# Performance work log

Measured on AMD Instinct MI355X. Metric: run time of the kernel, lower is better.

Reference implementation:

```python
import jax, jax.numpy as jnp
import numpy as np

V, D, NH, L, T, B = 32000, 1024, 16, 6, 1024, 2
HS = D // NH
EPS = 1e-5


def setup_inputs() -> dict:
    key = jax.random.key(0)
    ks = jax.random.split(key, 20)
    s = 0.02
    inp = {
        'tokens': jax.random.randint(ks[0], (B, T), 0, V),
        'tok_emb': jax.random.normal(ks[1], (V, D), jnp.float32) * s,
        'pos_emb': jax.random.normal(ks[2], (T, D), jnp.float32) * s,
        'Wq': jax.random.normal(ks[3], (L, D, NH, HS), jnp.float32) * s,
        'Wk': jax.random.normal(ks[4], (L, D, NH, HS), jnp.float32) * s,
        'Wv': jax.random.normal(ks[5], (L, D, NH, HS), jnp.float32) * s,
        'Wo': jax.random.normal(ks[6], (L, D, D), jnp.float32) * s,
        'bo': jnp.zeros((L, D), jnp.float32),
        'ln1_s': jnp.ones((L, D), jnp.float32),
        'ln1_b': jnp.zeros((L, D), jnp.float32),
        'ln2_s': jnp.ones((L, D), jnp.float32),
        'ln2_b': jnp.zeros((L, D), jnp.float32),
        'W1': jax.random.normal(ks[7], (L, D, 4 * D), jnp.float32) * s,
        'b1': jnp.zeros((L, 4 * D), jnp.float32),
        'W2': jax.random.normal(ks[8], (L, 4 * D, D), jnp.float32) * s,
        'b2': jnp.zeros((L, D), jnp.float32),
        'lnf_s': jnp.ones((D,), jnp.float32),
        'lnf_b': jnp.zeros((D,), jnp.float32),
        'Wlm': jax.random.normal(ks[9], (D, V), jnp.float32) * s,
        'blm': jnp.zeros((V,), jnp.float32),
    }
    return inp


def _layernorm(x, scale, bias):
    m = jnp.mean(x, axis=-1, keepdims=True)
    v = jnp.mean(jnp.square(x - m), axis=-1, keepdims=True)
    return (x - m) * jax.lax.rsqrt(v + EPS) * scale + bias


def reference(tokens, tok_emb, pos_emb, Wq, Wk, Wv, Wo, bo,
              ln1_s, ln1_b, ln2_s, ln2_b, W1, b1, W2, b2,
              lnf_s, lnf_b, Wlm, blm):
    x = tok_emb[tokens] + pos_emb[None, :, :]  # [B,T,D]
    causal = jnp.tril(jnp.ones((T, T), bool))
    scale = HS ** -0.5
    for l in range(L):
        h = _layernorm(x, ln1_s[l], ln1_b[l])
        q = jnp.einsum('btd,dhe->bhte', h, Wq[l])
        k = jnp.einsum('btd,dhe->bhte', h, Wk[l])
        v = jnp.einsum('btd,dhe->bhte', h, Wv[l])
        wei = jnp.einsum('bhqe,bhke->bhqk', q, k) * scale
        wei = jnp.where(causal, wei, -jnp.inf)
        wei = jax.nn.softmax(wei, axis=-1)
        attn = jnp.einsum('bhqk,bhke->bhqe', wei, v)  # [B,NH,T,HS]
        attn = attn.transpose(0, 2, 1, 3).reshape(B, T, D)
        x = x + attn @ Wo[l] + bo[l]
        h = _layernorm(x, ln2_s[l], ln2_b[l])
        x = x + jax.nn.relu(h @ W1[l] + b1[l]) @ W2[l] + b2[l]
    x = _layernorm(x, lnf_s, lnf_b)
    logits = x @ Wlm + blm  # [B,T,V]
    return logits
```

## Files before the change

### kernel.cpp

```cpp
#include <hip/hip_runtime.h>
#include <hip/hip_bf16.h>
#include <stdint.h>

#define L_LAYERS 6
#define D_MODEL  1024
#define N_HEAD   16
#define H_SZ     64
#define T_SEQ    1024
#define B_BATCH  2
#define M_ROWS   2048
#define V_VOCAB  32000

typedef __attribute__((ext_vector_type(8))) short bf16x8;
typedef __attribute__((ext_vector_type(4))) short bf16x4;
typedef __attribute__((ext_vector_type(4))) float floatx4;

static __device__ __forceinline__ short f2bf(float f) {
  __hip_bfloat16 h = __float2bfloat16(f);
  return *reinterpret_cast<short*>(&h);
}
static __device__ __forceinline__ float bf2f(short s) {
  unsigned u = ((unsigned)(unsigned short)s) << 16;
  return *reinterpret_cast<float*>(&u);
}

static __device__ __forceinline__ void lds_cp16(const void* g, void* l) {
  __builtin_amdgcn_global_load_lds(
      (const __attribute__((address_space(1))) uint32_t*)g,
      (__attribute__((address_space(3))) uint32_t*)l, 16, 0, 0);
}

#define WVM(n) asm volatile("s_waitcnt vmcnt(" #n ")" ::: "memory")
#define BARR __builtin_amdgcn_s_barrier()

__global__ __launch_bounds__(256) void transpose_cvt(const float* __restrict__ in,
                                                     short* __restrict__ out,
                                                     int R, int C,
                                                     long in_stride, long out_stride) {
  in  += (size_t)blockIdx.z * in_stride;
  out += (size_t)blockIdx.z * out_stride;
  __shared__ float tile[64][65];
  int rt = blockIdx.x, ct = blockIdx.y;
  int tid = threadIdx.x;
  int r0 = tid >> 4;
  int c0 = (tid & 15) << 2;
  const float* ip = in + (size_t)(rt * 64) * C + ct * 64;
#pragma unroll
  for (int p = 0; p < 4; ++p) {
    int r = r0 + (p << 4);
    float4 v = *(const float4*)(ip + (size_t)r * C + c0);
    tile[r][c0] = v.x; tile[r][c0 + 1] = v.y; tile[r][c0 + 2] = v.z; tile[r][c0 + 3] = v.w;
  }
  __syncthreads();
  short* op = out + (size_t)(ct * 64) * R + rt * 64;
#pragma unroll
  for (int p = 0; p < 2; ++p) {
    int c = (tid >> 3) + (p << 5);
    int r8 = (tid & 7) << 3;
    bf16x8 o8;
#pragma unroll
    for (int j = 0; j < 8; ++j) o8[j] = f2bf(tile[r8 + j][c]);
    *(bf16x8*)(op + (size_t)c * R + r8) = o8;
  }
}

__global__ __launch_bounds__(256) void embedln_kernel(const int* __restrict__ tokens,
                                                      const float* __restrict__ tok_emb,
                                                      const float* __restrict__ pos_emb,
                                                      float* __restrict__ x,
                                                      const float* __restrict__ sc,
                                                      const float* __restrict__ bi,
                                                      short* __restrict__ out) {
  int row = blockIdx.x, tid = threadIdx.x;
  int t = row & 1023;
  int tok = tokens[row];
  int c = tid << 2;
  float4 e = *(const float4*)(tok_emb + (size_t)tok * 1024 + c);
  float4 p = *(const float4*)(pos_emb + (size_t)t * 1024 + c);
  float4 v; v.x = e.x + p.x; v.y = e.y + p.y; v.z = e.z + p.z; v.w = e.w + p.w;
  *(float4*)(x + (size_t)row * 1024 + c) = v;
  float s = v.x + v.y + v.z + v.w;
  float q = v.x * v.x + v.y * v.y + v.z * v.z + v.w * v.w;
#pragma unroll
  for (int off = 32; off > 0; off >>= 1) {
    s += __shfl_xor(s, off);
    q += __shfl_xor(q, off);
  }
  __shared__ float rs[4], rq[4];
  if ((tid & 63) == 0) { rs[tid >> 6] = s; rq[tid >> 6] = q; }
  __syncthreads();
  s = rs[0] + rs[1] + rs[2] + rs[3];
  q = rq[0] + rq[1] + rq[2] + rq[3];
  float mean = s * (1.f / 1024.f);
  float var = q * (1.f / 1024.f) - mean * mean;
  float rstd = rsqrtf(var + 1e-5f);
  float4 g = *(const float4*)(sc + c);
  float4 bb = *(const float4*)(bi + c);
  bf16x4 o4;
  o4.x = f2bf((v.x - mean) * rstd * g.x + bb.x);
  o4.y = f2bf((v.y - mean) * rstd * g.y + bb.y);
  o4.z = f2bf((v.z - mean) * rstd * g.z + bb.z);
  o4.w = f2bf((v.w - mean) * rstd * g.w + bb.w);
  *(bf16x4*)(out + (size_t)row * 1024 + c) = o4;
}

__global__ __launch_bounds__(256) void lnred_kernel(float* __restrict__ xio,
                                                    const short* __restrict__ P0,
                                                    const short* __restrict__ P1,
                                                    const float* __restrict__ gb,
                                                    const float* __restrict__ sc,
                                                    const float* __restrict__ bi,
                                                    short* __restrict__ out) {
  int row = blockIdx.x, tid = threadIdx.x;
  int c = tid << 2;
  size_t base = (size_t)row * 1024 + c;
  float4 v = *(const float4*)(xio + base);
  bf16x4 p0 = *(const bf16x4*)(P0 + base);
  bf16x4 p1 = *(const bf16x4*)(P1 + base);
  float4 gv = *(const float4*)(gb + c);
  v.x += bf2f(p0.x) + bf2f(p1.x) + gv.x;
  v.y += bf2f(p0.y) + bf2f(p1.y) + gv.y;
  v.z += bf2f(p0.z) + bf2f(p1.z) + gv.z;
  v.w += bf2f(p0.w) + bf2f(p1.w) + gv.w;
  *(float4*)(xio + base) = v;
  float s = v.x + v.y + v.z + v.w;
  float q = v.x * v.x + v.y * v.y + v.z * v.z + v.w * v.w;
#pragma unroll
  for (int off = 32; off > 0; off >>= 1) {
    s += __shfl_xor(s, off);
    q += __shfl_xor(q, off);
  }
  __shared__ float rs[4], rq[4];
  if ((tid & 63) == 0) { rs[tid >> 6] = s; rq[tid >> 6] = q; }
  __syncthreads();
  s = rs[0] + rs[1] + rs[2] + rs[3];
  q = rq[0] + rq[1] + rq[2] + rq[3];
  float mean = s * (1.f / 1024.f);
  float var = q * (1.f / 1024.f) - mean * mean;
  float rstd = rsqrtf(var + 1e-5f);
  float4 g = *(const float4*)(sc + c);
  float4 bb = *(const float4*)(bi + c);
  bf16x4 o4;
  o4.x = f2bf((v.x - mean) * rstd * g.x + bb.x);
  o4.y = f2bf((v.y - mean) * rstd * g.y + bb.y);
  o4.z = f2bf((v.z - mean) * rstd * g.z + bb.z);
  o4.w = f2bf((v.w - mean) * rstd * g.w + bb.w);
  *(bf16x4*)(out + (size_t)row * 1024 + c) = o4;
}

__global__ __launch_bounds__(256) void lnred4_kernel(float* __restrict__ xio,
                                                     const short* __restrict__ P01,
                                                     const short* __restrict__ P23,
                                                     const float* __restrict__ gb,
                                                     const float* __restrict__ sc,
                                                     const float* __restrict__ bi,
                                                     short* __restrict__ out) {
  const size_t MN = (size_t)M_ROWS * 1024;
  int row = blockIdx.x, tid = threadIdx.x;
  int c = tid << 2;
  size_t base = (size_t)row * 1024 + c;
  float4 v = *(const float4*)(xio + base);
  bf16x4 p0 = *(const bf16x4*)(P01 + base);
  bf16x4 p1 = *(const bf16x4*)(P01 + MN + base);
  bf16x4 p2 = *(const bf16x4*)(P23 + base);
  bf16x4 p3 = *(const bf16x4*)(P23 + MN + base);
  float4 gv = *(const float4*)(gb + c);
  v.x += bf2f(p0.x) + bf2f(p1.x) + bf2f(p2.x) + bf2f(p3.x) + gv.x;
  v.y += bf2f(p0.y) + bf2f(p1.y) + bf2f(p2.y) + bf2f(p3.y) + gv.y;
  v.z += bf2f(p0.z) + bf2f(p1.z) + bf2f(p2.z) + bf2f(p3.z) + gv.z;
  v.w += bf2f(p0.w) + bf2f(p1.w) + bf2f(p2.w) + bf2f(p3.w) + gv.w;
  *(float4*)(xio + base) = v;
  float s = v.x + v.y + v.z + v.w;
  float q = v.x * v.x + v.y * v.y + v.z * v.z + v.w * v.w;
#pragma unroll
  for (int off = 32; off > 0; off >>= 1) {
    s += __shfl_xor(s, off);
    q += __shfl_xor(q, off);
  }
  __shared__ float rs[4], rq[4];
  if ((tid & 63) == 0) { rs[tid >> 6] = s; rq[tid >> 6] = q; }
  __syncthreads();
  s = rs[0] + rs[1] + rs[2] + rs[3];
  q = rq[0] + rq[1] + rq[2] + rq[3];
  float mean = s * (1.f / 1024.f);
  float var = q * (1.f / 1024.f) - mean * mean;
  float rstd = rsqrtf(var + 1e-5f);
  float4 g = *(const float4*)(sc + c);
  float4 bb = *(const float4*)(bi + c);
  bf16x4 o4;
  o4.x = f2bf((v.x - mean) * rstd * g.x + bb.x);
  o4.y = f2bf((v.y - mean) * rstd * g.y + bb.y);
  o4.z = f2bf((v.z - mean) * rstd * g.z + bb.z);
  o4.w = f2bf((v.w - mean) * rstd * g.w + bb.w);
  *(bf16x4*)(out + (size_t)row * 1024 + c) = o4;
}

__global__ __launch_bounds__(256) void gemm3sk_kernel(const short* __restrict__ A,
                                                      const short* __restrict__ Bt,
                                                      short* __restrict__ Pout,
                                                      int K, int N) {
  constexpr int ABY = 64 * 128;
  constexpr int BBY = 128 * 128;
  extern __shared__ char smem[];
  char* Asm = smem;
  char* Bsm = smem + 3 * ABY;
  const int NB = N >> 7;
  int nwg = 64 * NB;
  int bid = blockIdx.x;
  int wgid = (bid & 7) * (nwg >> 3) + (bid >> 3);
  int half = wgid >= (nwg >> 1);
  int w2 = wgid - half * (nwg >> 1);
  int bn = w2 >> 5, bm = w2 & 31;
  int kbase = half * (K >> 1);
  Pout += (size_t)half * M_ROWS * N;
  int tid = threadIdx.x;
  int lane = tid & 63, w = tid >> 6;
  int lr = lane & 15, lg = lane >> 4;
  int wn = w & 1, wm = w >> 1;

  const floatx4 FZ = {0.f, 0.f, 0.f, 0.f};
  floatx4 acc[2][4];
#pragma unroll
  for (int m = 0; m < 2; ++m)
#pragma unroll
    for (int n = 0; n < 4; ++n) acc[m][n] = FZ;

  size_t aoff[2], boff[4];
  {
    int rr = tid >> 3;
    int g = (tid & 7) ^ (rr & 7);
#pragma unroll
    for (int i = 0; i < 2; ++i)
      aoff[i] = (size_t)(bm * 64 + i * 32 + rr) * K + kbase + g * 8;
#pragma unroll
    for (int i = 0; i < 4; ++i)
      boff[i] = (size_t)(bn * 128 + i * 32 + rr) * K + kbase + g * 8;
  }

#define STA3(b, k0)                                                        \
  _Pragma("unroll") for (int i = 0; i < 2; ++i)                            \
    lds_cp16(A + aoff[i] + (k0), Asm + (b) * ABY + i * 4096 + tid * 16);
#define STB3(b, k0)                                                        \
  _Pragma("unroll") for (int i = 0; i < 4; ++i)                            \
    lds_cp16(Bt + boff[i] + (k0), Bsm + (b) * BBY + i * 4096 + tid * 16);
#define LDA3(b, kh)                                                        \
  _Pragma("unroll") for (int f = 0; f < 2; ++f) {                          \
    int lrow = wm * 32 + f * 16 + lr;                                      \
    af[f] = *(const bf16x8*)(Asm + (b) * ABY + lrow * 128 +                \
                             (((((kh) << 2) + lg) ^ (lrow & 7)) << 4));    \
  }
#define LDB3(b, kh)                                                        \
  _Pragma("unroll") for (int n = 0; n < 4; ++n) {                          \
    int lcol = wn * 64 + n * 16 + lr;                                      \
    bfr[n] = *(const bf16x8*)(Bsm + (b) * BBY + lcol * 128 +               \
                              (((((kh) << 2) + lg) ^ (lcol & 7)) << 4));   \
  }
#define MFMA3                                                              \
  __builtin_amdgcn_s_setprio(1);                                           \
  _Pragma("unroll") for (int f = 0; f < 2; ++f)                            \
  _Pragma("unroll") for (int n = 0; n < 4; ++n)                            \
    acc[f][n] = __builtin_amdgcn_mfma_f32_16x16x32_bf16(af[f], bfr[n],     \
                                                        acc[f][n], 0, 0, 0);\
  __builtin_amdgcn_s_setprio(0);

  const int nt = (K >> 1) >> 6;
  STA3(0, 0); STB3(0, 0);
  STA3(1, 64); STB3(1, 64);
  WVM(6);
  BARR;

  int cbuf = 0, sbuf = 2;
  for (int t = 0; t < nt; ++t) {
    bf16x8 af[2], bfr[4];
    bool pre = (t + 2 < nt);
    int k2 = (t + 2) << 6;
    if (pre) { STA3(sbuf, k2); }
    LDA3(cbuf, 0); LDB3(cbuf, 0);
    MFMA3;
    if (pre) { STB3(sbuf, k2); }
    LDA3(cbuf, 1); LDB3(cbuf, 1);
    MFMA3;
    if (pre) { WVM(6); } else { WVM(0); }
    BARR;
    cbuf = (cbuf == 2) ? 0 : cbuf + 1;
    sbuf = (sbuf == 2) ? 0 : sbuf + 1;
  }

#pragma unroll
  for (int n = 0; n < 4; ++n) {
    int col = (bn << 7) + wn * 64 + (n << 4) + lr;
#pragma unroll
    for (int m = 0; m < 2; ++m) {
      int row0 = bm * 64 + wm * 32 + (m << 4) + (lg << 2);
#pragma unroll
      for (int r = 0; r < 4; ++r)
        Pout[(size_t)(row0 + r) * N + col] = f2bf(acc[m][n][r]);
    }
  }
#undef STA3
#undef STB3
#undef LDA3
#undef LDB3
#undef MFMA3
}

template <bool BIAS, bool RELU, bool OUTBF16, bool VSPLIT>
__global__ __launch_bounds__(512) void gemmw_kernel(const short* __restrict__ A,
                                                    const short* __restrict__ Bt,
                                                    const float* __restrict__ bias,
                                                    void* __restrict__ Cout,
                                                    short* __restrict__ vtb,
                                                    int K, int N) {
  constexpr int ABY = 128 * 128;
  constexpr int BBY = 256 * 128;
  extern __shared__ char smem[];
  char* Asm = smem;
  char* Bsm = smem + 3 * ABY;
  const int NB = N >> 8;
  int nwg = 16 * NB;
  int bid = blockIdx.x;
  int wgid = (bid & 7) * (nwg >> 3) + (bid >> 3);
  int bn = wgid >> 4, bm = wgid & 15;
  int tid = threadIdx.x;
  int lane = tid & 63, w = tid >> 6;
  int lr = lane & 15, lg = lane >> 4;
  int wm = w >> 2, wn = w & 3;

  const floatx4 FZ = {0.f, 0.f, 0.f, 0.f};
  floatx4 acc[4][4];
#pragma unroll
  for (int m = 0; m < 4; ++m)
#pragma unroll
    for (int n = 0; n < 4; ++n) acc[m][n] = FZ;

  size_t aoff[2], boff[4];
  {
    int rr = tid >> 3;
    int g = (tid & 7) ^ (rr & 7);
#pragma unroll
    for (int i = 0; i < 2; ++i)
      aoff[i] = (size_t)(bm * 128 + i * 64 + rr) * K + g * 8;
#pragma unroll
    for (int i = 0; i < 4; ++i)
      boff[i] = (size_t)(bn * 256 + i * 64 + rr) * K + g * 8;
  }

#define STAW(b, k0)                                                        \
  _Pragma("unroll") for (int i = 0; i < 2; ++i)                            \
    lds_cp16(A + aoff[i] + (k0), Asm + (b) * ABY + i * 8192 + tid * 16);
#define STBW(b, k0)                                                        \
  _Pragma("unroll") for (int i = 0; i < 4; ++i)                            \
    lds_cp16(Bt + boff[i] + (k0), Bsm + (b) * BBY + i * 8192 + tid * 16);
#define LDAW(b, kh)                                                        \
  _Pragma("unroll") for (int f = 0; f < 4; ++f) {                          \
    int lrow = wm * 64 + f * 16 + lr;                                      \
    af[f] = *(const bf16x8*)(Asm + (b) * ABY + lrow * 128 +                \
                             (((((kh) << 2) + lg) ^ (lrow & 7)) << 4));    \
  }
#define LDBW(b, kh)                                                        \
  _Pragma("unroll") for (int n = 0; n < 4; ++n) {                          \
    int lcol = wn * 64 + n * 16 + lr;                                      \
    bfr[n] = *(const bf16x8*)(Bsm + (b) * BBY + lcol * 128 +               \
                              (((((kh) << 2) + lg) ^ (lcol & 7)) << 4));   \
  }
#define MFMAW                                                              \
  __builtin_amdgcn_s_setprio(1);                                           \
  _Pragma("unroll") for (int f = 0; f < 4; ++f)                            \
  _Pragma("unroll") for (int n = 0; n < 4; ++n)                            \
    acc[f][n] = __builtin_amdgcn_mfma_f32_16x16x32_bf16(af[f], bfr[n],     \
                                                        acc[f][n], 0, 0, 0);\
  __builtin_amdgcn_s_setprio(0);

  const int nt = K >> 6;
  STAW(0, 0); STBW(0, 0);
  STAW(1, 64); STBW(1, 64);
  WVM(6);
  BARR;

  int cbuf = 0, sbuf = 2;
  for (int t = 0; t < nt; ++t) {
    bf16x8 af[4], bfr[4];
    bool pre = (t + 2 < nt);
    int k2 = (t + 2) << 6;
    if (pre) { STAW(sbuf, k2); }
    LDAW(cbuf, 0); LDBW(cbuf, 0);
    MFMAW;
    if (pre) { STBW(sbuf, k2); }
    LDAW(cbuf, 1); LDBW(cbuf, 1);
    MFMAW;
    if (pre) { WVM(6); } else { WVM(0); }
    BARR;
    cbuf = (cbuf == 2) ? 0 : cbuf + 1;
    sbuf = (sbuf == 2) ? 0 : sbuf + 1;
  }

#pragma unroll
  for (int n = 0; n < 4; ++n) {
    int col = (bn << 8) + wn * 64 + (n << 4) + lr;
    float bv = 0.f;
    if (BIAS) bv = bias[col];
#pragma unroll
    for (int m = 0; m < 4; ++m) {
      int row0 = bm * 128 + wm * 64 + (m << 4) + (lg << 2);
      if (VSPLIT && col >= 2048) {
        int hc = col - 2048;
        int brow = row0 >> 10, t0 = row0 & 1023;
        ushort4 pk;
        pk.x = (unsigned short)f2bf(acc[m][n][0]);
        pk.y = (unsigned short)f2bf(acc[m][n][1]);
        pk.z = (unsigned short)f2bf(acc[m][n][2]);
        pk.w = (unsigned short)f2bf(acc[m][n][3]);
        *(ushort4*)(vtb + ((size_t)(((brow << 4) + (hc >> 6)) << 6) + (hc & 63)) * 1024 + t0) = pk;
      } else {
#pragma unroll
        for (int r = 0; r < 4; ++r) {
          size_t idx = (size_t)(row0 + r) * N + col;
          float val = acc[m][n][r] + bv;
          if (RELU) val = fmaxf(val, 0.f);
          if (OUTBF16) ((short*)Cout)[idx] = f2bf(val);
          else ((float*)Cout)[idx] = val;
        }
      }
    }
  }
#undef STAW
#undef STBW
#undef LDAW
#undef LDBW
#undef MFMAW
}

__global__ __launch_bounds__(512) void gemmwsk_kernel(const short* __restrict__ A,
                                                      const short* __restrict__ Bt,
                                                      short* __restrict__ P01,
                                                      short* __restrict__ P23,
                                                      int K, int N) {
  constexpr int ABY = 128 * 128;
  constexpr int BBY = 256 * 128;
  extern __shared__ char smem[];
  char* Asm = smem;
  char* Bsm = smem + 3 * ABY;
  const int NB = N >> 8;
  int nwg = 16 * NB * 4;
  int bid = blockIdx.x;
  int wgid = (bid & 7) * (nwg >> 3) + (bid >> 3);
  int per = nwg >> 2;
  int part = wgid / per;
  int w2 = wgid - part * per;
  int bn = w2 >> 4, bm = w2 & 15;
  int kbase = part * (K >> 2);
  short* Pout = (part < 2 ? P01 + (size_t)part * M_ROWS * N
                          : P23 + (size_t)(part - 2) * M_ROWS * N);
  int tid = threadIdx.x;
  int lane = tid & 63, w = tid >> 6;
  int lr = lane & 15, lg = lane >> 4;
  int wm = w >> 2, wn = w & 3;

  const floatx4 FZ = {0.f, 0.f, 0.f, 0.f};
  floatx4 acc[4][4];
#pragma unroll
  for (int m = 0; m < 4; ++m)
#pragma unroll
    for (int n = 0; n < 4; ++n) acc[m][n] = FZ;

  size_t aoff[2], boff[4];
  {
    int rr = tid >> 3;
    int g = (tid & 7) ^ (rr & 7);
#pragma unroll
    for (int i = 0; i < 2; ++i)
      aoff[i] = (size_t)(bm * 128 + i * 64 + rr) * K + kbase + g * 8;
#pragma unroll
    for (int i = 0; i < 4; ++i)
      boff[i] = (size_t)(bn * 256 + i * 64 + rr) * K + kbase + g * 8;
  }

#define STAW(b, k0)                                                        \
  _Pragma("unroll") for (int i = 0; i < 2; ++i)                            \
    lds_cp16(A + aoff[i] + (k0), Asm + (b) * ABY + i * 8192 + tid * 16);
#define STBW(b, k0)                                                        \
  _Pragma("unroll") for (int i = 0; i < 4; ++i)                            \
    lds_cp16(Bt + boff[i] + (k0), Bsm + (b) * BBY + i * 8192 + tid * 16);
#define LDAW(b, kh)                                                        \
  _Pragma("unroll") for (int f = 0; f < 4; ++f) {                          \
    int lrow = wm * 64 + f * 16 + lr;                                      \
    af[f] = *(const bf16x8*)(Asm + (b) * ABY + lrow * 128 +                \
                             (((((kh) << 2) + lg) ^ (lrow & 7)) << 4));    \
  }
#define LDBW(b, kh)                                                        \
  _Pragma("unroll") for (int n = 0; n < 4; ++n) {                          \
    int lcol = wn * 64 + n * 16 + lr;                                      \
    bfr[n] = *(const bf16x8*)(Bsm + (b) * BBY + lcol * 128 +               \
                              (((((kh) << 2) + lg) ^ (lcol & 7)) << 4));   \
  }
#define MFMAW                                                              \
  __builtin_amdgcn_s_setprio(1);                                           \
  _Pragma("unroll") for (int f = 0; f < 4; ++f)                            \
  _Pragma("unroll") for (int n = 0; n < 4; ++n)                            \
    acc[f][n] = __builtin_amdgcn_mfma_f32_16x16x32_bf16(af[f], bfr[n],     \
                                                        acc[f][n], 0, 0, 0);\
  __builtin_amdgcn_s_setprio(0);

  const int nt = (K >> 2) >> 6;
  STAW(0, 0); STBW(0, 0);
  STAW(1, 64); STBW(1, 64);
  WVM(6);
  BARR;

  int cbuf = 0, sbuf = 2;
  for (int t = 0; t < nt; ++t) {
    bf16x8 af[4], bfr[4];
    bool pre = (t + 2 < nt);
    int k2 = (t + 2) << 6;
    if (pre) { STAW(sbuf, k2); }
    LDAW(cbuf, 0); LDBW(cbuf, 0);
    MFMAW;
    if (pre) { STBW(sbuf, k2); }
    LDAW(cbuf, 1); LDBW(cbuf, 1);
    MFMAW;
    if (pre) { WVM(6); } else { WVM(0); }
    BARR;
    cbuf = (cbuf == 2) ? 0 : cbuf + 1;
    sbuf = (sbuf == 2) ? 0 : sbuf + 1;
  }

#pragma unroll
  for (int n = 0; n < 4; ++n) {
    int col = (bn << 8) + wn * 64 + (n << 4) + lr;
#pragma unroll
    for (int m = 0; m < 4; ++m) {
      int row0 = bm * 128 + wm * 64 + (m << 4) + (lg << 2);
#pragma unroll
      for (int r = 0; r < 4; ++r)
        Pout[(size_t)(row0 + r) * N + col] = f2bf(acc[m][n][r]);
    }
  }
#undef STAW
#undef STBW
#undef LDAW
#undef LDBW
#undef MFMAW
}

template <bool BIAS, bool OUTBF16>
__global__ __launch_bounds__(512) void gemm8_kernel(const short* __restrict__ A,
                                                    const short* __restrict__ Bt,
                                                    const float* __restrict__ bias,
                                                    void* __restrict__ Cout,
                                                    int K, int N) {
  extern __shared__ char smem[];
  char* Asm = smem;
  char* Bsm = smem + 65536;
  const int NB = N >> 8;
  int nwg = 8 * NB;
  int bid = blockIdx.x;
  int wgid = (bid & 7) * (nwg >> 3) + (bid >> 3);
  int bm = wgid & 7, bn = wgid >> 3;
  int tid = threadIdx.x;
  int lane = tid & 63, w = tid >> 6;
  int lr = lane & 15, lg = lane >> 4;
  int wm = w >> 2, wn = w & 3;

  const floatx4 FZ = {0.f, 0.f, 0.f, 0.f};
  floatx4 acc[8][4];
#pragma unroll
  for (int m = 0; m < 8; ++m)
#pragma unroll
    for (int n = 0; n < 4; ++n) acc[m][n] = FZ;

  size_t aoff[2][2], boff[4];
  {
    int rr = tid >> 3;
    int g = (tid & 7) ^ (rr & 7);
#pragma unroll
    for (int c = 0; c < 2; ++c)
#pragma unroll
      for (int i = 0; i < 2; ++i) {
        int lrow = i * 64 + rr;
        int grow = (lrow & 63) + ((lrow >> 6) << 7) + (c << 6);
        aoff[c][i] = (size_t)(bm * 256 + grow) * K + g * 8;
      }
#pragma unroll
    for (int i = 0; i < 4; ++i)
      boff[i] = (size_t)(bn * 256 + i * 64 + rr) * K + g * 8;
  }

  bf16x8 areg[4], breg[2][4];

#define LDA8(chunk, kh)                                                          \
  _Pragma("unroll") for (int f = 0; f < 4; ++f) {                                \
    int lrow = wm * 64 + f * 16 + lr;                                            \
    areg[f] = *(const bf16x8*)(Asm + buf * 32768 + (chunk) * 16384 + lrow * 128  \
                               + (((((kh) << 2) + lg) ^ (lrow & 7)) << 4));      \
  }
#define LDB8(kh)                                                                 \
  _Pragma("unroll") for (int n = 0; n < 4; ++n) {                                \
    int lcol = wn * 64 + n * 16 + lr;                                            \
    breg[kh][n] = *(const bf16x8*)(Bsm + buf * 32768 + lcol * 128                \
                                   + (((((kh) << 2) + lg) ^ (lcol & 7)) << 4));  \
  }
#define MFMA16(mh, kh)                                                           \
  __builtin_amdgcn_s_setprio(1);                                                 \
  _Pragma("unroll") for (int f = 0; f < 4; ++f)                                  \
  _Pragma("unroll") for (int n = 0; n < 4; ++n)                                  \
    acc[(mh) * 4 + f][n] = __builtin_amdgcn_mfma_f32_16x16x32_bf16(              \
        areg[f], breg[kh][n], acc[(mh) * 4 + f][n], 0, 0, 0);                    \
  __builtin_amdgcn_s_setprio(0);
#define STA8(chunk, dstbuf, k0)                                                  \
  _Pragma("unroll") for (int i = 0; i < 2; ++i)                                  \
    lds_cp16(A + aoff[chunk][i] + (k0),                                          \
             Asm + (dstbuf) * 32768 + (chunk) * 16384 + i * 8192 + tid * 16);
#define STB8(dstbuf, k0)                                                         \
  _Pragma("unroll") for (int i = 0; i < 4; ++i)                                  \
    lds_cp16(Bt + boff[i] + (k0),                                                \
             Bsm + (dstbuf) * 32768 + i * 8192 + tid * 16);

  const int nt = K >> 6;
  STA8(0, 0, 0); STB8(0, 0); STA8(1, 0, 0);
  WVM(2);
  BARR;

  int buf = 0;
  for (int t = 0; t < nt - 1; ++t) {
    int k1 = (t + 1) << 6;
    int ob = buf ^ 1;
    LDA8(0, 0); LDB8(0);
    STA8(0, ob, k1);
    BARR;
    MFMA16(0, 0);
    BARR;
    LDA8(0, 1); LDB8(1);
    STB8(ob, k1);
    WVM(6);
    BARR;
    MFMA16(0, 1);
    BARR;
    LDA8(1, 0);
    STA8(1, ob, k1);
    BARR;
    MFMA16(1, 0);
    BARR;
    LDA8(1, 1);
    WVM(2);
    BARR;
    MFMA16(1, 1);
    BARR;
    buf ^= 1;
  }
  LDA8(0, 0); LDB8(0);
  MFMA16(0, 0);
  LDA8(0, 1); LDB8(1);
  MFMA16(0, 1);
  WVM(0);
  BARR;
  LDA8(1, 0);
  MFMA16(1, 0);
  LDA8(1, 1);
  MFMA16(1, 1);

#pragma unroll
  for (int n = 0; n < 4; ++n) {
    int col = (bn << 8) + (wn << 6) + (n << 4) + lr;
    float bv = 0.f;
    if (BIAS) bv = bias[col];
#pragma unroll
    for (int m = 0; m < 8; ++m) {
      int row0 = (bm << 8) + (wm << 7) + (m << 4) + (lg << 2);
#pragma unroll
      for (int r = 0; r < 4; ++r) {
        size_t idx = (size_t)(row0 + r) * N + col;
        float val = acc[m][n][r] + bv;
        if (OUTBF16) ((short*)Cout)[idx] = f2bf(val);
        else ((float*)Cout)[idx] = val;
      }
    }
  }
#undef LDA8
#undef LDB8
#undef MFMA16
#undef STA8
#undef STB8
}

__global__ __launch_bounds__(256) void attn_kernel(const short* __restrict__ qkv,
                                                   const short* __restrict__ vt,
                                                   short* __restrict__ out) {
  int bh = blockIdx.x;
  int qt = blockIdx.y;
  int b = bh >> 4, hh = bh & 15;
  int tid = threadIdx.x;
  int lane = tid & 63, w = tid >> 6;
  int lr = lane & 15, lg = lane >> 4;

  __shared__ short Ks[128 * 64];
  __shared__ short Vs[64 * 128];
  __shared__ short Ps[4][16 * 132];

  const floatx4 FZ = {0.f, 0.f, 0.f, 0.f};
  const float C2 = 0.18033688f;
  const short* qb = qkv + (size_t)((b << 10) + (qt << 6) + (w << 4) + lr) * 3072 + (hh << 6);
  bf16x8 qf0 = *(const bf16x8*)(qb + (lg << 3));
  bf16x8 qf1 = *(const bf16x8*)(qb + 32 + (lg << 3));

  floatx4 o[4];
  float mrun[4], lrun[4];
#pragma unroll
  for (int r = 0; r < 4; ++r) { o[r] = FZ; mrun[r] = -3e38f; lrun[r] = 0.f; }

  int krow = tid >> 3, kgr = tid & 7;
  int vrow = tid >> 4, vgr = tid & 15;
  const short* kB = qkv + (size_t)(b << 10) * 3072 + 1024 + (hh << 6);
  const short* vB = vt + (size_t)(bh << 6) * 1024;

#define STKV(JT)                                                           \
  _Pragma("unroll") for (int i = 0; i < 4; ++i) {                          \
    int r = (i << 5) + krow;                                               \
    lds_cp16(kB + (size_t)(((JT) << 7) + r) * 3072 + ((kgr ^ (r & 7)) << 3), \
             (char*)Ks + i * 4096 + tid * 16);                             \
  }                                                                        \
  _Pragma("unroll") for (int i = 0; i < 4; ++i) {                          \
    int r = (i << 4) + vrow;                                               \
    lds_cp16(vB + (size_t)r * 1024 + ((JT) << 7) + ((vgr ^ (r & 15)) << 3), \
             (char*)Vs + i * 4096 + tid * 16);                             \
  }

#define CHUNK_COMPUTE(NF, MASK, JT)                                        \
  {                                                                        \
    const char* KsB = (const char*)Ks;                                     \
    const char* VsB = (const char*)Vs;                                     \
    floatx4 s[NF];                                                         \
    _Pragma("unroll") for (int f = 0; f < NF; ++f) {                       \
      int rk = (f << 4) + lr;                                              \
      int sw = rk & 7;                                                     \
      bf16x8 kf0 = *(const bf16x8*)(KsB + rk * 128 + ((lg ^ sw) << 4));    \
      bf16x8 kf1 = *(const bf16x8*)(KsB + rk * 128 + (((4 + lg) ^ sw) << 4)); \
      floatx4 t0 = __builtin_amdgcn_mfma_f32_16x16x32_bf16(qf0, kf0, FZ, 0, 0, 0); \
      s[f] = __builtin_amdgcn_mfma_f32_16x16x32_bf16(qf1, kf1, t0, 0, 0, 0); \
    }                                                                      \
    int qrow0 = (qt << 6) + (w << 4) + (lg << 2);                          \
    _Pragma("unroll") for (int f = 0; f < NF; ++f)                         \
    _Pragma("unroll") for (int r = 0; r < 4; ++r) {                        \
      float sv = s[f][r] * C2;                                             \
      if (MASK && (((JT) << 7) + (f << 4) + lr > qrow0 + r)) sv = -3e38f;  \
      s[f][r] = sv;                                                        \
    }                                                                      \
    float mt[4] = {-3e38f, -3e38f, -3e38f, -3e38f};                        \
    _Pragma("unroll") for (int f = 0; f < NF; ++f)                         \
    _Pragma("unroll") for (int r = 0; r < 4; ++r) mt[r] = fmaxf(mt[r], s[f][r]); \
    _Pragma("unroll") for (int off = 1; off < 16; off <<= 1)               \
    _Pragma("unroll") for (int r = 0; r < 4; ++r)                          \
      mt[r] = fmaxf(mt[r], __shfl_xor(mt[r], off));                        \
    float corr[4], psum[4];                                                \
    _Pragma("unroll") for (int r = 0; r < 4; ++r) {                        \
      float mnew = fmaxf(mrun[r], mt[r]);                                  \
      corr[r] = exp2f(mrun[r] - mnew);                                     \
      mrun[r] = mnew;                                                      \
      float ps = 0.f;                                                      \
      _Pragma("unroll") for (int f = 0; f < NF; ++f) {                     \
        float e = exp2f(s[f][r] - mnew);                                   \
        s[f][r] = e;                                                       \
        ps += e;                                                           \
      }                                                                    \
      psum[r] = ps;                                                        \
    }                                                                      \
    _Pragma("unroll") for (int off = 1; off < 16; off <<= 1)               \
    _Pragma("unroll") for (int r = 0; r < 4; ++r)                          \
      psum[r] += __shfl_xor(psum[r], off);                                 \
    floatx4 cv;                                                            \
    _Pragma("unroll") for (int r = 0; r < 4; ++r) {                        \
      lrun[r] = lrun[r] * corr[r] + psum[r];                               \
      cv[r] = corr[r];                                                     \
    }                                                                      \
    _Pragma("unroll") for (int f = 0; f < 4; ++f) o[f] *= cv;              \
    char* PsB = (char*)&Ps[w][0];                                          \
    _Pragma("unroll") for (int f = 0; f < NF; ++f)                         \
    _Pragma("unroll") for (int r = 0; r < 4; ++r)                          \
      *(short*)(PsB + ((lg << 2) + r) * 264 + (((f << 4) + lr) << 1)) =    \
          f2bf(s[f][r]);                                                   \
    _Pragma("unroll") for (int kk = 0; kk < (NF >> 1); ++kk) {             \
      const char* pb = PsB + lr * 264 + (kk << 6) + (lg << 4);             \
      union { struct { bf16x4 lo, hi; } h2; bf16x8 v; } pu;                \
      pu.h2.lo = *(const bf16x4*)pb;                                       \
      pu.h2.hi = *(const bf16x4*)(pb + 8);                                 \
      bf16x8 pa = pu.v;                                                    \
      _Pragma("unroll") for (int f = 0; f < 4; ++f) {                      \
        int rv = (f << 4) + lr;                                            \
        bf16x8 vf = *(const bf16x8*)(VsB + rv * 256 +                      \
                                     ((((kk << 2) + lg) ^ (rv & 15)) << 4)); \
        o[f] = __builtin_amdgcn_mfma_f32_16x16x32_bf16(pa, vf, o[f], 0, 0, 0); \
      }                                                                    \
    }                                                                      \
  }

  const int nfull = qt >> 1;
  for (int jt = 0; jt < nfull; ++jt) {
    STKV(jt);
    WVM(0);
    BARR;
    CHUNK_COMPUTE(8, false, jt)
    BARR;
  }
  STKV(nfull);
  WVM(0);
  BARR;
  if (qt & 1) {
    CHUNK_COMPUTE(8, true, nfull)
  } else {
    CHUNK_COMPUTE(4, true, nfull)
  }
#undef STKV
#undef CHUNK_COMPUTE

#pragma unroll
  for (int f = 0; f < 4; ++f) {
#pragma unroll
    for (int r = 0; r < 4; ++r) {
      int row = (qt << 6) + (w << 4) + (lg << 2) + r;
      int col = (hh << 6) + (f << 4) + lr;
      out[(size_t)((b << 10) + row) * 1024 + col] = f2bf(o[f][r] / lrun[r]);
    }
  }
}

extern "C" void kernel_launch(void* const* d_in, const int* in_sizes, int n_in,
                              void* d_out, int out_size, void* d_ws, size_t ws_size,
                              hipStream_t stream) {
  const int*   tokens  = (const int*)d_in[0];
  const float* tok_emb = (const float*)d_in[1];
  const float* pos_emb = (const float*)d_in[2];
  const float* Wq  = (const float*)d_in[3];
  const float* Wk  = (const float*)d_in[4];
  const float* Wv  = (const float*)d_in[5];
  const float* Wo  = (const float*)d_in[6];
  const float* bo  = (const float*)d_in[7];
  const float* ln1s = (const float*)d_in[8];
  const float* ln1b = (const float*)d_in[9];
  const float* ln2s = (const float*)d_in[10];
  const float* ln2b = (const float*)d_in[11];
  const float* W1  = (const float*)d_in[12];
  const float* b1  = (const float*)d_in[13];
  const float* W2  = (const float*)d_in[14];
  const float* b2  = (const float*)d_in[15];
  const float* lnfs = (const float*)d_in[16];
  const float* lnfb = (const float*)d_in[17];
  const float* Wlm = (const float*)d_in[18];
  const float* blm = (const float*)d_in[19];

  short* wqkvT = (short*)d_ws;
  short* woT   = wqkvT + (size_t)L_LAYERS * 3072 * 1024;
  short* w1T   = woT   + (size_t)L_LAYERS * 1024 * 1024;
  short* w2T   = w1T   + (size_t)L_LAYERS * 4096 * 1024;
  short* wlmT  = w2T   + (size_t)L_LAYERS * 1024 * 4096;
  float* x     = (float*)(wlmT + (size_t)V_VOCAB * 1024);
  short* h     = (short*)(x + (size_t)M_ROWS * 1024);
  short* qkv   = h + (size_t)M_ROWS * 1024;
  short* vtb   = qkv + (size_t)M_ROWS * 3072;
  short* attnb = vtb + (size_t)B_BATCH * N_HEAD * H_SZ * T_SEQ;
  short* mid   = attnb + (size_t)M_ROWS * 1024;
  short* psum  = mid + (size_t)M_ROWS * 4096;
  short* psum1 = psum + (size_t)M_ROWS * 1024;
  short* psum23 = qkv;

  dim3 blk(256, 1, 1);

  (void)hipFuncSetAttribute(reinterpret_cast<const void*>(&gemm8_kernel<true, false>),
                            hipFuncAttributeMaxDynamicSharedMemorySize, 131072);
  (void)hipFuncSetAttribute(reinterpret_cast<const void*>(&gemm3sk_kernel),
                            hipFuncAttributeMaxDynamicSharedMemorySize, 73728);
  (void)hipFuncSetAttribute(reinterpret_cast<const void*>(&gemmw_kernel<false, false, true, true>),
                            hipFuncAttributeMaxDynamicSharedMemorySize, 147456);
  (void)hipFuncSetAttribute(reinterpret_cast<const void*>(&gemmw_kernel<true, true, true, false>),
                            hipFuncAttributeMaxDynamicSharedMemorySize, 147456);
  (void)hipFuncSetAttribute(reinterpret_cast<const void*>(&gemmwsk_kernel),
                            hipFuncAttributeMaxDynamicSharedMemorySize, 147456);

  transpose_cvt<<<dim3(16, 16, 6), blk, 0, stream>>>(Wq, wqkvT,             1024, 1024, 1048576, 3072 * 1024);
  transpose_cvt<<<dim3(16, 16, 6), blk, 0, stream>>>(Wk, wqkvT + 1048576,   1024, 1024, 1048576, 3072 * 1024);
  transpose_cvt<<<dim3(16, 16, 6), blk, 0, stream>>>(Wv, wqkvT + 2097152,   1024, 1024, 1048576, 3072 * 1024);
  transpose_cvt<<<dim3(16, 16, 6), blk, 0, stream>>>(Wo, woT,               1024, 1024, 1048576, 1048576);
  transpose_cvt<<<dim3(16, 64, 6), blk, 0, stream>>>(W1, w1T,               1024, 4096, 4194304, 4194304);
  transpose_cvt<<<dim3(64, 16, 6), blk, 0, stream>>>(W2, w2T,               4096, 1024, 4194304, 4194304);
  transpose_cvt<<<dim3(16, 500, 1), blk, 0, stream>>>(Wlm, wlmT,            1024, V_VOCAB, 0, 0);

  embedln_kernel<<<M_ROWS, blk, 0, stream>>>(tokens, tok_emb, pos_emb, x, ln1s, ln1b, h);

  for (int l = 0; l < L_LAYERS; ++l) {
    if (l > 0) {
      lnred4_kernel<<<M_ROWS, blk, 0, stream>>>(x, psum, psum23, b2 + (l - 1) * 1024,
                                                ln1s + l * 1024, ln1b + l * 1024, h);
    }
    gemmw_kernel<false, false, true, true><<<16 * 12, dim3(512, 1, 1), 147456, stream>>>(
        h, wqkvT + (size_t)l * 3072 * 1024, nullptr, qkv, vtb, 1024, 3072);
    attn_kernel<<<dim3(32, 16), blk, 0, stream>>>(qkv, vtb, attnb);
    gemm3sk_kernel<<<64 * 8, blk, 73728, stream>>>(
        attnb, woT + (size_t)l * 1048576, psum, 1024, 1024);
    lnred_kernel<<<M_ROWS, blk, 0, stream>>>(x, psum, psum1, bo + l * 1024,
                                             ln2s + l * 1024, ln2b + l * 1024, h);
    gemmw_kernel<true, true, true, false><<<16 * 16, dim3(512, 1, 1), 147456, stream>>>(
        h, w1T + (size_t)l * 4194304, b1 + l * 4096, mid, nullptr, 1024, 4096);
    gemmwsk_kernel<<<16 * 16, dim3(512, 1, 1), 147456, stream>>>(
        mid, w2T + (size_t)l * 4194304, psum, psum23, 4096, 1024);
  }

  lnred4_kernel<<<M_ROWS, blk, 0, stream>>>(x, psum, psum23, b2 + 5 * 1024,
                                            lnfs, lnfb, h);
  gemm8_kernel<true, false><<<dim3(8 * 125), dim3(512, 1, 1), 131072, stream>>>(
      h, wlmT, blm, (float*)d_out, 1024, V_VOCAB);
}
```

Measured before the change: 1.006 ms.

## Split long causal attention query tiles across two blocks with merge kernel

The attention kernel now splits the key range of the later query tiles (8-15) across two blocks, each storing unnormalized partial outputs with the running max and sum in float scratch. A new merge kernel combines the two partials with a log-sum-exp rescale and writes the bf16 output. The aim is to balance the causal workload and raise the block count from 512 to 768. The cost is an extra kernel launch plus the float partial traffic through scratch that reuses the MLP mid buffer.

Result: no change. 1.001 ms (median of 2 runs) (-0.6%).

```diff
diff --git a/kernel.cpp b/kernel.cpp
--- a/kernel.cpp
+++ b/kernel.cpp
@@ -684,9 +684,24 @@
 
 __global__ __launch_bounds__(256) void attn_kernel(const short* __restrict__ qkv,
                                                    const short* __restrict__ vt,
-                                                   short* __restrict__ out) {
+                                                   short* __restrict__ out,
+                                                   float* __restrict__ po,
+                                                   float* __restrict__ pm,
+                                                   float* __restrict__ pl) {
   int bh = blockIdx.x;
-  int qt = blockIdx.y;
+  int y = blockIdx.y;
+  int qt, c0, cend, half = 0;
+  bool whole, epi;
+  if (y < 8) {
+    qt = y; whole = true; c0 = 0; cend = qt >> 1; epi = true;
+  } else {
+    int idx = y - 8;
+    qt = 8 + (idx >> 1); half = idx & 1; whole = false;
+    int nfull = qt >> 1;
+    int h0 = (nfull + 1) >> 1;
+    if (half == 0) { c0 = 0; cend = h0; epi = false; }
+    else           { c0 = h0; cend = nfull; epi = true; }
+  }
   int b = bh >> 4, hh = bh & 15;
   int tid = threadIdx.x;
   int lane = tid & 63, w = tid >> 6;
@@ -792,33 +807,89 @@
     }                                                                      \
   }
 
-  const int nfull = qt >> 1;
-  for (int jt = 0; jt < nfull; ++jt) {
+  for (int jt = c0; jt < cend; ++jt) {
     STKV(jt);
     WVM(0);
     BARR;
     CHUNK_COMPUTE(8, false, jt)
     BARR;
   }
-  STKV(nfull);
-  WVM(0);
-  BARR;
-  if (qt & 1) {
-    CHUNK_COMPUTE(8, true, nfull)
-  } else {
-    CHUNK_COMPUTE(4, true, nfull)
+  if (epi) {
+    int je = qt >> 1;
+    STKV(je);
+    WVM(0);
+    BARR;
+    if (qt & 1) {
+      CHUNK_COMPUTE(8, true, je)
+    } else {
+      CHUNK_COMPUTE(4, true, je)
+    }
   }
 #undef STKV
 #undef CHUNK_COMPUTE
 
-#pragma unroll
-  for (int f = 0; f < 4; ++f) {
-#pragma unroll
-    for (int r = 0; r < 4; ++r) {
-      int row = (qt << 6) + (w << 4) + (lg << 2) + r;
-      int col = (hh << 6) + (f << 4) + lr;
-      out[(size_t)((b << 10) + row) * 1024 + col] = f2bf(o[f][r] / lrun[r]);
+  if (whole) {
+#pragma unroll
+    for (int f = 0; f < 4; ++f) {
+#pragma unroll
+      for (int r = 0; r < 4; ++r) {
+        int row = (qt << 6) + (w << 4) + (lg << 2) + r;
+        int col = (hh << 6) + (f << 4) + lr;
+        out[(size_t)((b << 10) + row) * 1024 + col] = f2bf(o[f][r] / lrun[r]);
+      }
     }
+  } else {
+    int qtp = qt - 8;
+    size_t pb = (((size_t)bh * 8 + qtp) * 2 + half) << 12;
+#pragma unroll
+    for (int f = 0; f < 4; ++f) {
+#pragma unroll
+      for (int r = 0; r < 4; ++r) {
+        int row = (w << 4) + (lg << 2) + r;
+        int col = (f << 4) + lr;
+        po[pb + row * 64 + col] = o[f][r];
+      }
+    }
+    if (lr == 0) {
+      int mi = (int)((((bh * 8 + qtp) << 1) + half) << 6);
+#pragma unroll
+      for (int r = 0; r < 4; ++r) {
+        int row = (w << 4) + (lg << 2) + r;
+        pm[mi + row] = mrun[r];
+        pl[mi + row] = lrun[r];
+      }
+    }
+  }
+}
+
+__global__ __launch_bounds__(256) void attnmerge_kernel(const float* __restrict__ po,
+                                                        const float* __restrict__ pm,
+                                                        const float* __restrict__ pl,
+                                                        short* __restrict__ out) {
+  int bh = blockIdx.x, y = blockIdx.y;
+  int qt = 8 + y;
+  int b = bh >> 4, hh = bh & 15;
+  int tid = threadIdx.x;
+  int row = tid >> 2, cg = tid & 3;
+  size_t base0 = ((((size_t)bh * 8 + y) * 2) << 12) + row * 64;
+  size_t base1 = base0 + 4096;
+  int mi = (((bh * 8 + y) << 1) << 6) + row;
+  float m0 = pm[mi], l0 = pl[mi];
+  float m1 = pm[mi + 64], l1 = pl[mi + 64];
+  float M = fmaxf(m0, m1);
+  float w0 = exp2f(m0 - M), w1 = exp2f(m1 - M);
+  float inv = 1.f / (l0 * w0 + l1 * w1);
+  short* op = out + (size_t)((b << 10) + (qt << 6) + row) * 1024 + (hh << 6) + (cg << 4);
+#pragma unroll
+  for (int p = 0; p < 4; ++p) {
+    float4 a = *(const float4*)(po + base0 + (cg << 4) + (p << 2));
+    float4 c = *(const float4*)(po + base1 + (cg << 4) + (p << 2));
+    bf16x4 o4;
+    o4.x = f2bf((a.x * w0 + c.x * w1) * inv);
+    o4.y = f2bf((a.y * w0 + c.y * w1) * inv);
+    o4.z = f2bf((a.z * w0 + c.z * w1) * inv);
+    o4.w = f2bf((a.w * w0 + c.w * w1) * inv);
+    *(bf16x4*)(op + (p << 2)) = o4;
   }
 }
 
@@ -860,6 +931,9 @@
   short* psum  = mid + (size_t)M_ROWS * 4096;
   short* psum1 = psum + (size_t)M_ROWS * 1024;
   short* psum23 = qkv;
+  float* apo = (float*)mid;
+  float* apm = apo + (size_t)32 * 8 * 2 * 64 * 64;
+  float* apl = apm + 32 * 8 * 2 * 64;
 
   dim3 blk(256, 1, 1);
 
@@ -891,7 +965,8 @@
     }
     gemmw_kernel<false, false, true, true><<<16 * 12, dim3(512, 1, 1), 147456, stream>>>(
         h, wqkvT + (size_t)l * 3072 * 1024, nullptr, qkv, vtb, 1024, 3072);
-    attn_kernel<<<dim3(32, 16), blk, 0, stream>>>(qkv, vtb, attnb);
+    attn_kernel<<<dim3(32, 24), blk, 0, stream>>>(qkv, vtb, attnb, apo, apm, apl);
+    attnmerge_kernel<<<dim3(32, 8), blk, 0, stream>>>(apo, apm, apl, attnb);
     gemm3sk_kernel<<<64 * 8, blk, 73728, stream>>>(
         attnb, woT + (size_t)l * 1048576, psum, 1024, 1024);
     lnred_kernel<<<M_ROWS, blk, 0, stream>>>(x, psum, psum1, bo + l * 1024,
```
